# Optimization experiments

Hardware: AMD Instinct MI355X
Metric: run time of the kernel (lower is better)

Reference implementation:

```python
import jax, jax.numpy as jnp
import numpy as np

EPS = 0.1
MAX_ITER = 100
THRESH = 0.1


def setup_inputs() -> dict:
    key = jax.random.key(0)
    k1, k2, k3, k4 = jax.random.split(key, 4)
    N, P1, P2, D = 4, 1024, 1024, 16
    x = jax.random.normal(k1, (N, P1, D), dtype=jnp.float32)
    y = jax.random.normal(k2, (N, P2, D), dtype=jnp.float32)
    wx = jax.random.uniform(k3, (N, P1), dtype=jnp.float32)
    wy = jax.random.uniform(k4, (N, P2), dtype=jnp.float32)
    # normalize to probability weights (typical usage for empirical measures)
    wx = wx / jnp.sum(wx, axis=-1, keepdims=True)
    wy = wy / jnp.sum(wy, axis=-1, keepdims=True)
    return {"x": x, "y": y, "wx": wx, "wy": wy}


def _cost_matrix(x, y):
    # |x_i - y_j|^1 summed over feature dim -> [N, P1, P2]
    return jnp.sum(jnp.abs(x[:, :, None, :] - y[:, None, :, :]), axis=-1)


def reference(x, y, wx, wy):
    C = _cost_matrix(x, y)                     # [N, P1, P2]
    mu, nu = wx, wy                            # [N, P1], [N, P2]
    log_mu = jnp.log(mu + 1e-8)
    log_nu = jnp.log(nu + 1e-8)

    def M(u, v):
        # (-C_ij + u_i + v_j) / eps
        return (-C + u[:, :, None] + v[:, None, :]) / EPS

    def step(carry, _):
        u, v, done = carry
        u_new = EPS * (log_mu - jax.nn.logsumexp(M(u, v), axis=-1)) + u
        v_new = EPS * (log_nu - jax.nn.logsumexp(M(u_new, v), axis=-2)) + v
        err = jnp.mean(jnp.sum(jnp.abs(u_new - u), axis=-1))
        # emulate torch's early break: freeze u,v once converged
        u_out = jnp.where(done, u, u_new)
        v_out = jnp.where(done, v, v_new)
        done = done | (err < THRESH)
        return (u_out, v_out, done), None

    u0 = jnp.zeros_like(mu)
    v0 = jnp.zeros_like(nu)
    (u, v, _), _ = jax.lax.scan(step, (u0, v0, jnp.array(False)), None, length=MAX_ITER)

    pi = jnp.exp(M(u, v))                      # transport plan [N, P1, P2]
    cost = jnp.sum(pi * C, axis=(-2, -1))      # [N]  (reduction='none')
    return cost, pi, C
```

## Files before the change

kernel.cpp:

```cpp
#include <hip/hip_runtime.h>

static constexpr int   NB      = 4;
static constexpr int   PP      = 1024;
static constexpr int   DD      = 16;
static constexpr float EPSV    = 0.1f;
static constexpr float KE      = 14.42695041f;
static constexpr float KL      = 0.0693147181f;
static constexpr int   MAXIT   = 100;
static constexpr float THRESHV = 0.1f;

static constexpr int NBLK = 256;
static constexpr int NTHR = 512;
static constexpr unsigned DONEG = 1000000u;

__device__ __forceinline__ float fexp2(float v) { return __builtin_amdgcn_exp2f(v); }
__device__ __forceinline__ float flog2(float v) { return __builtin_amdgcn_logf(v); }

static constexpr int    ERR_F_OFF     = 4352;
static constexpr size_t WS_ZERO_BYTES = 4352 * 4;
static constexpr size_t ERR_BYTES    = 512 * 4;

static constexpr int VSNAP_OFF = 131072;

__device__ __forceinline__ float aload(const float* p) {
    return __hip_atomic_load(p, __ATOMIC_RELAXED, __HIP_MEMORY_SCOPE_AGENT);
}
__device__ __forceinline__ void astore(float* p, float v) {
    __hip_atomic_store(p, v, __ATOMIC_RELAXED, __HIP_MEMORY_SCOPE_AGENT);
}
__device__ __forceinline__ unsigned aloadu(const unsigned* p) {
    return __hip_atomic_load(p, __ATOMIC_RELAXED, __HIP_MEMORY_SCOPE_AGENT);
}
__device__ __forceinline__ void astoreu(unsigned* p, unsigned v) {
    __hip_atomic_store(p, v, __ATOMIC_RELAXED, __HIP_MEMORY_SCOPE_AGENT);
}
__device__ __forceinline__ float2 aload2(const float* p) {
    unsigned long long v = __hip_atomic_load((const unsigned long long*)p,
                                             __ATOMIC_RELAXED, __HIP_MEMORY_SCOPE_AGENT);
    union { unsigned long long u; float f[2]; } c; c.u = v;
    return make_float2(c.f[0], c.f[1]);
}
__device__ __forceinline__ void astore2(float* p, float a, float b) {
    union { unsigned long long u; float f[2]; } c; c.f[0] = a; c.f[1] = b;
    __hip_atomic_store((unsigned long long*)p, c.u,
                       __ATOMIC_RELAXED, __HIP_MEMORY_SCOPE_AGENT);
}

__device__ __forceinline__ void gbar_group(unsigned* ws32, int n, int g, unsigned gen) {
    __syncthreads();
    if (threadIdx.x < 64) {
        if (threadIdx.x == 0) astoreu(ws32 + (n * 64 + g) * 16, gen);
        const unsigned* sp = ws32 + (n * 64 + threadIdx.x) * 16;
        while (__ballot(aloadu(sp) >= gen) != ~0ull)
            __builtin_amdgcn_s_sleep(1);
    }
    __syncthreads();
}

__global__ __launch_bounds__(NTHR, 2)
void sinkhorn_kernel(const float* __restrict__ x, const float* __restrict__ y,
                     const float* __restrict__ wx, const float* __restrict__ wy,
                     float* __restrict__ out, float* __restrict__ ws)
{
    __shared__ float rt[16 * PP];
    __shared__ float sbuf[PP];
    __shared__ float cred[8];
    __shared__ int   Ts;

    unsigned* ws32  = (unsigned*)ws;
    unsigned* Tslot = ws32 + 4096;
    unsigned* exitf = ws32 + 4104;
    float*    ews   = ws + ERR_F_OFF;

    float* out_cost = out;
    float* out_pi   = out + NB;
    float* out_C    = out + NB + (size_t)NB * PP * PP;

    const int b   = blockIdx.x;
    const int n   = b >> 6;
    const int g   = b & 63;
    const int i0  = g * 16;
    const int w   = threadIdx.x >> 6;
    const int l   = threadIdx.x & 63;
    const int tid = threadIdx.x;

    float* sc = out_C + (size_t)n * PP * PP;

    float4 xr[2][4];
    #pragma unroll
    for (int rr = 0; rr < 2; ++rr) {
        const float4* xp = (const float4*)(x + ((size_t)n * PP + (i0 + 2 * w + rr)) * DD);
        #pragma unroll
        for (int q = 0; q < 4; ++q) xr[rr][q] = xp[q];
    }
    #pragma unroll 4
    for (int k = 0; k < 16; ++k) {
        int j = l + 64 * k;
        const float4* yp = (const float4*)(y + ((size_t)n * PP + j) * DD);
        float4 y0 = yp[0], y1 = yp[1], y2 = yp[2], y3 = yp[3];
        #pragma unroll
        for (int rr = 0; rr < 2; ++rr) {
            float c = fabsf(xr[rr][0].x - y0.x) + fabsf(xr[rr][0].y - y0.y)
                    + fabsf(xr[rr][0].z - y0.z) + fabsf(xr[rr][0].w - y0.w)
                    + fabsf(xr[rr][1].x - y1.x) + fabsf(xr[rr][1].y - y1.y)
                    + fabsf(xr[rr][1].z - y1.z) + fabsf(xr[rr][1].w - y1.w)
                    + fabsf(xr[rr][2].x - y2.x) + fabsf(xr[rr][2].y - y2.y)
                    + fabsf(xr[rr][2].z - y2.z) + fabsf(xr[rr][2].w - y2.w)
                    + fabsf(xr[rr][3].x - y3.x) + fabsf(xr[rr][3].y - y3.y)
                    + fabsf(xr[rr][3].z - y3.z) + fabsf(xr[rr][3].w - y3.w);
            rt[(2 * w + rr) * PP + j] = c;
        }
    }

    float4 yc[2][4];
    #pragma unroll
    for (int c = 0; c < 2; ++c) {
        const float4* yp = (const float4*)(y + ((size_t)n * PP + (i0 + 2 * w + c)) * DD);
        #pragma unroll
        for (int q = 0; q < 4; ++q) yc[c][q] = yp[q];
    }
    float2 c2[16];
    #pragma unroll 4
    for (int k = 0; k < 16; ++k) {
        const float4* xp = (const float4*)(x + ((size_t)n * PP + (l + 64 * k)) * DD);
        float4 x0 = xp[0], x1 = xp[1], x2 = xp[2], x3 = xp[3];
        float cc[2];
        #pragma unroll
        for (int c = 0; c < 2; ++c) {
            cc[c] = fabsf(x0.x - yc[c][0].x) + fabsf(x0.y - yc[c][0].y)
                  + fabsf(x0.z - yc[c][0].z) + fabsf(x0.w - yc[c][0].w)
                  + fabsf(x1.x - yc[c][1].x) + fabsf(x1.y - yc[c][1].y)
                  + fabsf(x1.z - yc[c][1].z) + fabsf(x1.w - yc[c][1].w)
                  + fabsf(x2.x - yc[c][2].x) + fabsf(x2.y - yc[c][2].y)
                  + fabsf(x2.z - yc[c][2].z) + fabsf(x2.w - yc[c][2].w)
                  + fabsf(x3.x - yc[c][3].x) + fabsf(x3.y - yc[c][3].y)
                  + fabsf(x3.z - yc[c][3].z) + fabsf(x3.w - yc[c][3].w);
        }
        c2[k] = make_float2(cc[0], cc[1]);
    }

    float lmu[2], lnu[2];
    #pragma unroll
    for (int rr = 0; rr < 2; ++rr) {
        lmu[rr] = __logf(wx[n * PP + i0 + 2 * w + rr] + 1e-8f);
        lnu[rr] = __logf(wy[n * PP + i0 + 2 * w + rr] + 1e-8f);
    }

    float uprev0 = 0.f, uprev1 = 0.f;

    #pragma unroll 1
    for (int t = 0; t < MAXIT; ++t) {
        if (t >= 2) {
            unsigned ef = aloadu(exitf + n);
            if (ef != 0u && t >= (int)ef + 1) break;
        }

        if (t == 0) {
            sbuf[2 * tid] = 0.f; sbuf[2 * tid + 1] = 0.f;
        } else {
            float2 vp = aload2(sc + VSNAP_OFF + (size_t)(t - 1) * PP + 2 * tid);
            sbuf[2 * tid] = vp.x; sbuf[2 * tid + 1] = vp.y;
        }
        __syncthreads();

        {
            float4 tt[2][4];
            float m0 = -3.4e38f, m1 = -3.4e38f;
            #pragma unroll
            for (int k = 0; k < 4; ++k) {
                int j = 256 * k + 4 * l;
                float4 v4 = *(const float4*)&sbuf[j];
                float4 ca = *(const float4*)&rt[(2 * w) * PP + j];
                float4 cb = *(const float4*)&rt[(2 * w + 1) * PP + j];
                tt[0][k] = make_float4(v4.x - ca.x, v4.y - ca.y, v4.z - ca.z, v4.w - ca.w);
                tt[1][k] = make_float4(v4.x - cb.x, v4.y - cb.y, v4.z - cb.z, v4.w - cb.w);
                m0 = fmaxf(m0, fmaxf(fmaxf(tt[0][k].x, tt[0][k].y), fmaxf(tt[0][k].z, tt[0][k].w)));
                m1 = fmaxf(m1, fmaxf(fmaxf(tt[1][k].x, tt[1][k].y), fmaxf(tt[1][k].z, tt[1][k].w)));
            }
            #pragma unroll
            for (int off = 32; off >= 1; off >>= 1) {
                m0 = fmaxf(m0, __shfl_xor(m0, off));
                m1 = fmaxf(m1, __shfl_xor(m1, off));
            }
            float s0 = 0.f, s1 = 0.f;
            #pragma unroll
            for (int k = 0; k < 4; ++k) {
                s0 += fexp2((tt[0][k].x - m0) * KE) + fexp2((tt[0][k].y - m0) * KE)
                    + fexp2((tt[0][k].z - m0) * KE) + fexp2((tt[0][k].w - m0) * KE);
                s1 += fexp2((tt[1][k].x - m1) * KE) + fexp2((tt[1][k].y - m1) * KE)
                    + fexp2((tt[1][k].z - m1) * KE) + fexp2((tt[1][k].w - m1) * KE);
            }
            #pragma unroll
            for (int off = 32; off >= 1; off >>= 1) {
                s0 += __shfl_xor(s0, off);
                s1 += __shfl_xor(s1, off);
            }
            float un0 = EPSV * lmu[0] - (m0 + KL * flog2(s0));
            float un1 = EPSV * lmu[1] - (m1 + KL * flog2(s1));
            if (l == 0) astore2(sc + (size_t)t * PP + i0 + 2 * w, un0, un1);
        }

        gbar_group(ws32, n, g, (unsigned)(2 * t + 1));

        {
            float2 up = aload2(sc + (size_t)t * PP + 2 * tid);
            sbuf[2 * tid] = up.x; sbuf[2 * tid + 1] = up.y;
            float we = fabsf(up.x - uprev0) + fabsf(up.y - uprev1);
            uprev0 = up.x; uprev1 = up.y;
            #pragma unroll
            for (int off = 32; off >= 1; off >>= 1) we += __shfl_xor(we, off);
            if (l == 0) cred[w] = we;
        }
        __syncthreads();

        {
            float tt0[16], tt1[16], m0 = -3.4e38f, m1 = -3.4e38f;
            #pragma unroll
            for (int k = 0; k < 16; ++k) {
                float uu = sbuf[l + 64 * k];
                tt0[k] = uu - c2[k].x;
                tt1[k] = uu - c2[k].y;
                m0 = fmaxf(m0, tt0[k]);
                m1 = fmaxf(m1, tt1[k]);
            }
            #pragma unroll
            for (int off = 32; off >= 1; off >>= 1) {
                m0 = fmaxf(m0, __shfl_xor(m0, off));
                m1 = fmaxf(m1, __shfl_xor(m1, off));
            }
            float s0 = 0.f, s1 = 0.f;
            #pragma unroll
            for (int k = 0; k < 16; ++k) {
                s0 += fexp2((tt0[k] - m0) * KE);
                s1 += fexp2((tt1[k] - m1) * KE);
            }
            #pragma unroll
            for (int off = 32; off >= 1; off >>= 1) {
                s0 += __shfl_xor(s0, off);
                s1 += __shfl_xor(s1, off);
            }
            float vn0 = EPSV * lnu[0] - (m0 + KL * flog2(s0));
            float vn1 = EPSV * lnu[1] - (m1 + KL * flog2(s1));
            if (l == 0)
                astore2(sc + VSNAP_OFF + (size_t)t * PP + i0 + 2 * w, vn0, vn1);
        }
        if (g == 0 && tid == 0) {
            float es = cred[0] + cred[1] + cred[2] + cred[3]
                     + cred[4] + cred[5] + cred[6] + cred[7];
            astore(ews + n * 128 + t, es);
        }

        __syncthreads();
        if (tid < 64) {
            if (tid == 0) astoreu(ws32 + (n * 64 + g) * 16, (unsigned)(2 * t + 2));
            if (g == 0) {
                float s1f = aload(ews + 0 * 128 + tid) + aload(ews + 1 * 128 + tid)
                          + aload(ews + 2 * 128 + tid) + aload(ews + 3 * 128 + tid);
                float s2f = aload(ews + 0 * 128 + 64 + tid) + aload(ews + 1 * 128 + 64 + tid)
                          + aload(ews + 2 * 128 + 64 + tid) + aload(ews + 3 * 128 + 64 + tid);
                unsigned long long bb = __ballot(s1f < THRESHV * (float)NB)
                                      | __ballot(s2f < THRESHV * (float)NB);
                if (bb != 0ull && tid == 0 && aloadu(exitf + n) == 0u)
                    astoreu(exitf + n, (unsigned)(t + 1));
            }
            const unsigned* sp = ws32 + (n * 64 + tid) * 16;
            while (__ballot(aloadu(sp) >= (unsigned)(2 * t + 2)) != ~0ull)
                __builtin_amdgcn_s_sleep(1);
        }
        __syncthreads();
    }

    if (g == 0 && tid == 0) astoreu(ws32 + (n * 64) * 16, DONEG);

    if (b == 0 && tid < 64) {
        for (;;) {
            bool ok = (tid >= 4) || (aloadu(ws32 + tid * 64 * 16) >= DONEG);
            if (__ballot(ok) == ~0ull) break;
            __builtin_amdgcn_s_sleep(2);
        }
        float s1f = aload(ews + 0 * 128 + tid) + aload(ews + 1 * 128 + tid)
                  + aload(ews + 2 * 128 + tid) + aload(ews + 3 * 128 + tid);
        float s2f = aload(ews + 0 * 128 + 64 + tid) + aload(ews + 1 * 128 + 64 + tid)
                  + aload(ews + 2 * 128 + 64 + tid) + aload(ews + 3 * 128 + 64 + tid);
        unsigned long long b1 = __ballot(s1f < THRESHV * (float)NB);
        unsigned long long b2 = __ballot(s2f < THRESHV * (float)NB);
        int T = b1 ? (__ffsll((long long)b1) - 1)
                   : (b2 ? 64 + (__ffsll((long long)b2) - 1) : MAXIT - 1);
        if (tid == 0) astoreu(Tslot, (unsigned)(T + 1));
    }
    if (tid == 0) {
        unsigned tv;
        while ((tv = aloadu(Tslot)) == 0u) __builtin_amdgcn_s_sleep(2);
        Ts = (int)tv - 1;
    }
    __syncthreads();
    const int T = Ts;

    float u_loc[2];
    {
        float2 up = aload2(sc + (size_t)T * PP + i0 + 2 * w);
        u_loc[0] = up.x; u_loc[1] = up.y;
        float2 vp = aload2(sc + VSNAP_OFF + (size_t)T * PP + 2 * tid);
        sbuf[2 * tid] = vp.x; sbuf[2 * tid + 1] = vp.y;
    }
    gbar_group(ws32, n, g, DONEG + 1u);

    float cacc = 0.f;
    #pragma unroll
    for (int rr = 0; rr < 2; ++rr) {
        int r = 2 * w + rr;
        int i = i0 + r;
        float un = u_loc[rr];
        #pragma unroll
        for (int k = 0; k < 4; ++k) {
            int j = 256 * k + 4 * l;
            float4 c4 = *(const float4*)&rt[r * PP + j];
            float4 v4 = *(const float4*)&sbuf[j];
            float4 p4;
            p4.x = fexp2((un + v4.x - c4.x) * KE);
            p4.y = fexp2((un + v4.y - c4.y) * KE);
            p4.z = fexp2((un + v4.z - c4.z) * KE);
            p4.w = fexp2((un + v4.w - c4.w) * KE);
            *(float4*)&out_pi[((size_t)n * PP + i) * PP + j] = p4;
            *(float4*)&out_C [((size_t)n * PP + i) * PP + j] = c4;
            cacc += p4.x * c4.x + p4.y * c4.y + p4.z * c4.z + p4.w * c4.w;
        }
    }
    #pragma unroll
    for (int off = 32; off >= 1; off >>= 1) cacc += __shfl_xor(cacc, off);
    if (l == 0) cred[w] = cacc;
    __syncthreads();
    if (tid == 0) {
        float s = 0.f;
        #pragma unroll
        for (int q = 0; q < 8; ++q) s += cred[q];
        atomicAdd(&out_cost[n], s);
    }
}

extern "C" void kernel_launch(void* const* d_in, const int* in_sizes, int n_in,
                              void* d_out, int out_size, void* d_ws, size_t ws_size,
                              hipStream_t stream) {
    const float* x  = (const float*)d_in[0];
    const float* y  = (const float*)d_in[1];
    const float* wx = (const float*)d_in[2];
    const float* wy = (const float*)d_in[3];
    float* out = (float*)d_out;
    float* ws  = (float*)d_ws;

    (void)hipMemsetAsync(d_ws, 0, WS_ZERO_BYTES, stream);
    (void)hipMemsetAsync((char*)d_ws + WS_ZERO_BYTES, 0x7f, ERR_BYTES, stream);
    (void)hipMemsetAsync(d_out, 0, NB * sizeof(float), stream);

    hipLaunchKernelGGL(sinkhorn_kernel, dim3(NBLK), dim3(NTHR), 0, stream,
                       x, y, wx, wy, out, ws);
}
```

Measured before the change: 787.3 us.

## Replace per-iteration group barriers with flag-in-data polling on encoded u/v

Removes the two per-iteration group barriers. Each u/v pair is stored XOR-encoded with a constant, so a zero or sentinel word means 'not yet written'. Consumers spin on the data itself, so each block waits only for the values it needs rather than for every block in the group. The in-loop early-exit check is dropped: all iterations now run, and the convergence step is still chosen at the end from the error history. The risks are extra iterations of work, and stale or uninitialised snapshot contents being mistaken for valid data, since readiness depends on the prior memory state.

```diff
diff --git a/kernel.cpp b/kernel.cpp
--- a/kernel.cpp
+++ b/kernel.cpp
@@ -16,11 +16,11 @@
 __device__ __forceinline__ float fexp2(float v) { return __builtin_amdgcn_exp2f(v); }
 __device__ __forceinline__ float flog2(float v) { return __builtin_amdgcn_logf(v); }
 
-static constexpr int    ERR_F_OFF     = 4352;
-static constexpr size_t WS_ZERO_BYTES = 4352 * 4;
-static constexpr size_t ERR_BYTES    = 512 * 4;
+static constexpr int    ERR_F_OFF = 4352;
+static constexpr size_t WS_BYTES  = (4352 + 512) * 4;
 
 static constexpr int VSNAP_OFF = 131072;
+static constexpr unsigned ENCX = 0x55555555u;
 
 __device__ __forceinline__ float aload(const float* p) {
     return __hip_atomic_load(p, __ATOMIC_RELAXED, __HIP_MEMORY_SCOPE_AGENT);
@@ -34,16 +34,23 @@
 __device__ __forceinline__ void astoreu(unsigned* p, unsigned v) {
     __hip_atomic_store(p, v, __ATOMIC_RELAXED, __HIP_MEMORY_SCOPE_AGENT);
 }
-__device__ __forceinline__ float2 aload2(const float* p) {
-    unsigned long long v = __hip_atomic_load((const unsigned long long*)p,
-                                             __ATOMIC_RELAXED, __HIP_MEMORY_SCOPE_AGENT);
-    union { unsigned long long u; float f[2]; } c; c.u = v;
-    return make_float2(c.f[0], c.f[1]);
-}
-__device__ __forceinline__ void astore2(float* p, float a, float b) {
-    union { unsigned long long u; float f[2]; } c; c.f[0] = a; c.f[1] = b;
+
+__device__ __forceinline__ void astore2enc(float* p, float a, float b) {
+    union { unsigned long long u; unsigned w[2]; float f[2]; } c;
+    c.f[0] = a; c.f[1] = b; c.w[0] ^= ENCX; c.w[1] ^= ENCX;
     __hip_atomic_store((unsigned long long*)p, c.u,
                        __ATOMIC_RELAXED, __HIP_MEMORY_SCOPE_AGENT);
+}
+__device__ __forceinline__ float2 poll2(const float* p) {
+    union { unsigned long long u; unsigned w[2]; float f[2]; } c;
+    for (;;) {
+        c.u = __hip_atomic_load((const unsigned long long*)p,
+                                __ATOMIC_RELAXED, __HIP_MEMORY_SCOPE_AGENT);
+        if (c.w[0] != 0u && c.w[0] != 0xAAAAAAAAu) break;
+        __builtin_amdgcn_s_sleep(1);
+    }
+    c.w[0] ^= ENCX; c.w[1] ^= ENCX;
+    return make_float2(c.f[0], c.f[1]);
 }
 
 __device__ __forceinline__ void gbar_group(unsigned* ws32, int n, int g, unsigned gen) {
@@ -69,7 +76,6 @@
 
     unsigned* ws32  = (unsigned*)ws;
     unsigned* Tslot = ws32 + 4096;
-    unsigned* exitf = ws32 + 4104;
     float*    ews   = ws + ERR_F_OFF;
 
     float* out_cost = out;
@@ -150,15 +156,10 @@
 
     #pragma unroll 1
     for (int t = 0; t < MAXIT; ++t) {
-        if (t >= 2) {
-            unsigned ef = aloadu(exitf + n);
-            if (ef != 0u && t >= (int)ef + 1) break;
-        }
-
         if (t == 0) {
             sbuf[2 * tid] = 0.f; sbuf[2 * tid + 1] = 0.f;
         } else {
-            float2 vp = aload2(sc + VSNAP_OFF + (size_t)(t - 1) * PP + 2 * tid);
+            float2 vp = poll2(sc + VSNAP_OFF + (size_t)(t - 1) * PP + 2 * tid);
             sbuf[2 * tid] = vp.x; sbuf[2 * tid + 1] = vp.y;
         }
         __syncthreads();
@@ -197,19 +198,20 @@
             }
             float un0 = EPSV * lmu[0] - (m0 + KL * flog2(s0));
             float un1 = EPSV * lmu[1] - (m1 + KL * flog2(s1));
-            if (l == 0) astore2(sc + (size_t)t * PP + i0 + 2 * w, un0, un1);
-        }
-
-        gbar_group(ws32, n, g, (unsigned)(2 * t + 1));
+            if (l == 0) astore2enc(sc + (size_t)t * PP + i0 + 2 * w, un0, un1);
+        }
+        __syncthreads();
 
         {
-            float2 up = aload2(sc + (size_t)t * PP + 2 * tid);
+            float2 up = poll2(sc + (size_t)t * PP + 2 * tid);
             sbuf[2 * tid] = up.x; sbuf[2 * tid + 1] = up.y;
-            float we = fabsf(up.x - uprev0) + fabsf(up.y - uprev1);
+            if (g == 0) {
+                float we = fabsf(up.x - uprev0) + fabsf(up.y - uprev1);
+                #pragma unroll
+                for (int off = 32; off >= 1; off >>= 1) we += __shfl_xor(we, off);
+                if (l == 0) cred[w] = we;
+            }
             uprev0 = up.x; uprev1 = up.y;
-            #pragma unroll
-            for (int off = 32; off >= 1; off >>= 1) we += __shfl_xor(we, off);
-            if (l == 0) cred[w] = we;
         }
         __syncthreads();
 
@@ -242,48 +244,35 @@
             float vn0 = EPSV * lnu[0] - (m0 + KL * flog2(s0));
             float vn1 = EPSV * lnu[1] - (m1 + KL * flog2(s1));
             if (l == 0)
-                astore2(sc + VSNAP_OFF + (size_t)t * PP + i0 + 2 * w, vn0, vn1);
+                astore2enc(sc + VSNAP_OFF + (size_t)t * PP + i0 + 2 * w, vn0, vn1);
         }
         if (g == 0 && tid == 0) {
             float es = cred[0] + cred[1] + cred[2] + cred[3]
                      + cred[4] + cred[5] + cred[6] + cred[7];
             astore(ews + n * 128 + t, es);
         }
-
         __syncthreads();
-        if (tid < 64) {
-            if (tid == 0) astoreu(ws32 + (n * 64 + g) * 16, (unsigned)(2 * t + 2));
-            if (g == 0) {
-                float s1f = aload(ews + 0 * 128 + tid) + aload(ews + 1 * 128 + tid)
-                          + aload(ews + 2 * 128 + tid) + aload(ews + 3 * 128 + tid);
-                float s2f = aload(ews + 0 * 128 + 64 + tid) + aload(ews + 1 * 128 + 64 + tid)
-                          + aload(ews + 2 * 128 + 64 + tid) + aload(ews + 3 * 128 + 64 + tid);
-                unsigned long long bb = __ballot(s1f < THRESHV * (float)NB)
-                                      | __ballot(s2f < THRESHV * (float)NB);
-                if (bb != 0ull && tid == 0 && aloadu(exitf + n) == 0u)
-                    astoreu(exitf + n, (unsigned)(t + 1));
-            }
-            const unsigned* sp = ws32 + (n * 64 + tid) * 16;
-            while (__ballot(aloadu(sp) >= (unsigned)(2 * t + 2)) != ~0ull)
-                __builtin_amdgcn_s_sleep(1);
-        }
-        __syncthreads();
-    }
-
-    if (g == 0 && tid == 0) astoreu(ws32 + (n * 64) * 16, DONEG);
+    }
+
+    if (tid == 0) astoreu(ws32 + (n * 64 + g) * 16, DONEG);
 
     if (b == 0 && tid < 64) {
         for (;;) {
-            bool ok = (tid >= 4) || (aloadu(ws32 + tid * 64 * 16) >= DONEG);
+            bool ok = (tid >= NB) || (aloadu(ws32 + (tid * 64) * 16) >= DONEG);
             if (__ballot(ok) == ~0ull) break;
             __builtin_amdgcn_s_sleep(2);
         }
         float s1f = aload(ews + 0 * 128 + tid) + aload(ews + 1 * 128 + tid)
                   + aload(ews + 2 * 128 + tid) + aload(ews + 3 * 128 + tid);
-        float s2f = aload(ews + 0 * 128 + 64 + tid) + aload(ews + 1 * 128 + 64 + tid)
-                  + aload(ews + 2 * 128 + 64 + tid) + aload(ews + 3 * 128 + 64 + tid);
-        unsigned long long b1 = __ballot(s1f < THRESHV * (float)NB);
-        unsigned long long b2 = __ballot(s2f < THRESHV * (float)NB);
+        bool c1 = (s1f < THRESHV * (float)NB);
+        bool c2v = false;
+        if (64 + tid < MAXIT) {
+            float s2f = aload(ews + 0 * 128 + 64 + tid) + aload(ews + 1 * 128 + 64 + tid)
+                      + aload(ews + 2 * 128 + 64 + tid) + aload(ews + 3 * 128 + 64 + tid);
+            c2v = (s2f < THRESHV * (float)NB);
+        }
+        unsigned long long b1 = __ballot(c1);
+        unsigned long long b2 = __ballot(c2v);
         int T = b1 ? (__ffsll((long long)b1) - 1)
                    : (b2 ? 64 + (__ffsll((long long)b2) - 1) : MAXIT - 1);
         if (tid == 0) astoreu(Tslot, (unsigned)(T + 1));
@@ -298,9 +287,9 @@
 
     float u_loc[2];
     {
-        float2 up = aload2(sc + (size_t)T * PP + i0 + 2 * w);
+        float2 up = poll2(sc + (size_t)T * PP + i0 + 2 * w);
         u_loc[0] = up.x; u_loc[1] = up.y;
-        float2 vp = aload2(sc + VSNAP_OFF + (size_t)T * PP + 2 * tid);
+        float2 vp = poll2(sc + VSNAP_OFF + (size_t)T * PP + 2 * tid);
         sbuf[2 * tid] = vp.x; sbuf[2 * tid + 1] = vp.y;
     }
     gbar_group(ws32, n, g, DONEG + 1u);
@@ -348,8 +337,7 @@
     float* out = (float*)d_out;
     float* ws  = (float*)d_ws;
 
-    (void)hipMemsetAsync(d_ws, 0, WS_ZERO_BYTES, stream);
-    (void)hipMemsetAsync((char*)d_ws + WS_ZERO_BYTES, 0x7f, ERR_BYTES, stream);
+    (void)hipMemsetAsync(d_ws, 0, WS_BYTES, stream);
     (void)hipMemsetAsync(d_out, 0, NB * sizeof(float), stream);
 
     hipLaunchKernelGGL(sinkhorn_kernel, dim3(NBLK), dim3(NTHR), 0, stream,
```

After: 816.9 us. 3.8% more time.
